# Kernel optimization log

Hardware: AMD Instinct MI355X
Metric: run time of the kernel (lower is better)

The kernel has to match this reference:

```python
import jax, jax.numpy as jnp
import numpy as np

B, S, H = 2, 2048, 512
N, D = 8, 64
EPS = 1e-6


def setup_inputs() -> dict:
    key = jax.random.key(0)
    ks = jax.random.split(key, 8)
    scale = 0.02
    return {
        "query": jax.random.normal(ks[0], (B, S, H), jnp.float32),
        "key": jax.random.normal(ks[1], (B, S, H), jnp.float32),
        "value": jax.random.normal(ks[2], (B, S, H), jnp.float32),
        "wq": jax.random.normal(ks[3], (H, N, D), jnp.float32) * scale,
        "bq": jnp.zeros((N, D), jnp.float32),
        "wk": jax.random.normal(ks[4], (H, N, D), jnp.float32) * scale,
        "bk": jnp.zeros((N, D), jnp.float32),
        "wv": jax.random.normal(ks[5], (H, N, D), jnp.float32) * scale,
        "bv": jnp.zeros((N, D), jnp.float32),
        "wo": jax.random.normal(ks[6], (N, D, H), jnp.float32) * scale,
        "bo": jnp.zeros((H,), jnp.float32),
        "step": 0,
    }


def _feature_map(x):
    # elu(x) + 1 (positive feature map for linear attention)
    return jax.nn.elu(x) + 1.0


def reference(query, key, value, wq, bq, wk, bk, wv, bv, wo, bo, step):
    # QKV projections: [B,S,H] -> [B,S,N,D]
    q = jnp.einsum('bsh,hnd->bsnd', query, wq) + bq
    k = jnp.einsum('bsh,hnd->bsnd', key, wk) + bk
    v = jnp.einsum('bsh,hnd->bsnd', value, wv) + bv

    phi_q = _feature_map(q)
    phi_k = _feature_map(k)

    b, s, n, d = k.shape
    # fold batch & heads: [S, B*N, D]
    pq = phi_q.transpose(1, 0, 2, 3).reshape(s, b * n, d)
    pk = phi_k.transpose(1, 0, 2, 3).reshape(s, b * n, d)
    vv = v.transpose(1, 0, 2, 3).reshape(s, b * n, d)

    # causal linear attention via prefix sums
    # state: cumulative sum of outer products phi_k v^T -> [S, B*N, D, D]
    st = jnp.cumsum(jnp.einsum('sbh,sbd->sbhd', pk, vv), axis=0)
    qs = jnp.einsum('sbhd,sbh->sbd', st, pq)
    z = jnp.cumsum(pk, axis=0)
    qz = jnp.einsum('sbh,sbh->sb', pq, z) + EPS
    a_v = qs / qz[..., None]
    a_v = a_v.transpose(1, 0, 2).reshape(b, s, n, d)

    # output projection: [B,S,N,D] -> [B,S,H]
    return jnp.einsum('bsnd,ndh->bsh', a_v, wo) + bo
```

## Files before the change

kernel.cpp:

```cpp
#include <hip/hip_runtime.h>
#include <hip/hip_bf16.h>
#include <cstdint>

#define B_    2
#define S_    2048
#define H_    512
#define N_    8
#define D_    64
#define BS_   4096
#define CHUNK 64
#define NCH   32
#define NBN   16
#define EPS_  1e-6f

typedef __attribute__((ext_vector_type(4))) float  f32x4;
typedef __attribute__((ext_vector_type(8))) short  short8;
typedef __attribute__((ext_vector_type(4))) short  short4_t;

static __device__ __forceinline__ unsigned short f2bf(float x) {
    __hip_bfloat16 h = __float2bfloat16(x);
    return *reinterpret_cast<unsigned short*>(&h);
}
static __device__ __forceinline__ float bf2f(unsigned short u) {
    unsigned int v = ((unsigned int)u) << 16;
    float f;
    __builtin_memcpy(&f, &v, 4);
    return f;
}

__global__ __launch_bounds__(256) void convert_act_kernel(
    const float* __restrict__ q, const float* __restrict__ k, const float* __restrict__ v,
    unsigned short* __restrict__ qb, unsigned short* __restrict__ kb, unsigned short* __restrict__ vb)
{
    const int p = blockIdx.y;
    const float* src = (p == 0) ? q : (p == 1) ? k : v;
    unsigned short* dst = (p == 0) ? qb : (p == 1) ? kb : vb;
    size_t idx = ((size_t)blockIdx.x * 256 + threadIdx.x) * 8;
    float4 a = *reinterpret_cast<const float4*>(src + idx);
    float4 b = *reinterpret_cast<const float4*>(src + idx + 4);
    short8 o;
    o[0] = (short)f2bf(a.x); o[1] = (short)f2bf(a.y);
    o[2] = (short)f2bf(a.z); o[3] = (short)f2bf(a.w);
    o[4] = (short)f2bf(b.x); o[5] = (short)f2bf(b.y);
    o[6] = (short)f2bf(b.z); o[7] = (short)f2bf(b.w);
    *reinterpret_cast<short8*>(dst + idx) = o;
}

__global__ __launch_bounds__(256) void convert_wt_kernel(
    const float* __restrict__ wq, const float* __restrict__ wk,
    const float* __restrict__ wv, const float* __restrict__ wo,
    unsigned short* __restrict__ wqt, unsigned short* __restrict__ wkt,
    unsigned short* __restrict__ wvt, unsigned short* __restrict__ wot)
{
    const int m = blockIdx.z;
    const float* W = (m == 0) ? wq : (m == 1) ? wk : (m == 2) ? wv : wo;
    unsigned short* Wt = (m == 0) ? wqt : (m == 1) ? wkt : (m == 2) ? wvt : wot;

    __shared__ float t[64][65];
    const int k0 = blockIdx.y * 64, c0 = blockIdx.x * 64;
    const int tid = threadIdx.x;
    const int rr = tid >> 6;
    const int cc = tid & 63;
#pragma unroll
    for (int p = 0; p < 16; p++) {
        int kl = rr + p * 4;
        t[kl][cc] = W[(size_t)(k0 + kl) * 512 + c0 + cc];
    }
    __syncthreads();
#pragma unroll
    for (int p = 0; p < 16; p++) {
        int cl = rr + p * 4;
        Wt[(size_t)(c0 + cl) * 512 + k0 + cc] = f2bf(t[cc][cl]);
    }
}

template<int MODE>
__device__ __forceinline__ void mfma_gemm_body(
    const unsigned short* __restrict__ X, const unsigned short* __restrict__ Wt,
    const float* __restrict__ bias,
    unsigned short* __restrict__ Obf, unsigned short* __restrict__ Ot,
    float* __restrict__ Of)
{
    __shared__ unsigned short As[128][72];
    __shared__ unsigned short Bs[128][72];

    const int tid  = threadIdx.x;
    const int lane = tid & 63;
    const int w    = tid >> 6;
    const int wm   = (w & 1) * 64;
    const int wn   = (w >> 1) * 64;
    const int row0 = blockIdx.y * 128;
    const int col0 = blockIdx.x * 128;
    const int frow = lane & 15;
    const int fk   = (lane >> 4) * 8;

    f32x4 acc[4][4];
#pragma unroll
    for (int m = 0; m < 4; m++)
#pragma unroll
        for (int n = 0; n < 4; n++) acc[m][n] = (f32x4){0.f, 0.f, 0.f, 0.f};

    const int lr = tid >> 3;
    const int lc = (tid & 7) * 8;

    for (int k0 = 0; k0 < 512; k0 += 64) {
#pragma unroll
        for (int p = 0; p < 4; p++) {
            int r = lr + p * 32;
            *reinterpret_cast<short8*>(&As[r][lc]) =
                *reinterpret_cast<const short8*>(X + (size_t)(row0 + r) * 512 + k0 + lc);
            *reinterpret_cast<short8*>(&Bs[r][lc]) =
                *reinterpret_cast<const short8*>(Wt + (size_t)(col0 + r) * 512 + k0 + lc);
        }
        __syncthreads();
#pragma unroll
        for (int kk = 0; kk < 64; kk += 32) {
            short8 a[4], b[4];
#pragma unroll
            for (int m = 0; m < 4; m++)
                a[m] = *reinterpret_cast<const short8*>(&As[wm + m * 16 + frow][kk + fk]);
#pragma unroll
            for (int n = 0; n < 4; n++)
                b[n] = *reinterpret_cast<const short8*>(&Bs[wn + n * 16 + frow][kk + fk]);
#pragma unroll
            for (int m = 0; m < 4; m++)
#pragma unroll
                for (int n = 0; n < 4; n++)
                    acc[m][n] = __builtin_amdgcn_mfma_f32_16x16x32_bf16(
                        a[m], b[n], acc[m][n], 0, 0, 0);
        }
        __syncthreads();
    }

#pragma unroll
    for (int n = 0; n < 4; n++) {
        int col = col0 + wn + n * 16 + frow;
        float bv_ = bias[col];
#pragma unroll
        for (int m = 0; m < 4; m++) {
            int rbase = row0 + wm + m * 16 + (lane >> 4) * 4;
            short4_t t4;
#pragma unroll
            for (int r = 0; r < 4; r++) {
                float val = acc[m][n][r] + bv_;
                if (MODE == 0 || MODE == 1)
                    val = (val > 0.f) ? (val + 1.f) : __expf(val);
                if (MODE == 3) {
                    Of[(size_t)(rbase + r) * 512 + col] = val;
                } else {
                    unsigned short ub = f2bf(val);
                    t4[r] = (short)ub;
                    if (MODE == 0 || MODE == 1)
                        Obf[(size_t)(rbase + r) * 512 + col] = ub;
                }
            }
            if (MODE == 1 || MODE == 2) {
                int bb = rbase >> 11;
                int t_ = rbase & 2047;
                *reinterpret_cast<short4_t*>(
                    Ot + (size_t)bb * (512 * 2048) + (size_t)col * 2048 + t_) = t4;
            }
        }
    }
}

__global__ __launch_bounds__(256) void qkv_proj_kernel(
    const unsigned short* __restrict__ qb, const unsigned short* __restrict__ kb,
    const unsigned short* __restrict__ vb,
    const unsigned short* __restrict__ wqt, const unsigned short* __restrict__ wkt,
    const unsigned short* __restrict__ wvt,
    const float* __restrict__ bq, const float* __restrict__ bk, const float* __restrict__ bv,
    unsigned short* __restrict__ pq, unsigned short* __restrict__ pk,
    unsigned short* __restrict__ pkT, unsigned short* __restrict__ pvT)
{
    int m = blockIdx.z;
    if (m == 0)      mfma_gemm_body<0>(qb, wqt, bq, pq, nullptr, nullptr);
    else if (m == 1) mfma_gemm_body<1>(kb, wkt, bk, pk, pkT, nullptr);
    else             mfma_gemm_body<2>(vb, wvt, bv, nullptr, pvT, nullptr);
}

__global__ __launch_bounds__(256) void out_proj_kernel(
    const unsigned short* __restrict__ avb, const unsigned short* __restrict__ wot,
    const float* __restrict__ bo, float* __restrict__ out)
{
    mfma_gemm_body<3>(avb, wot, bo, nullptr, nullptr, out);
}

__global__ __launch_bounds__(256) void chunk_kv_kernel(
    const unsigned short* __restrict__ pkT, const unsigned short* __restrict__ pvT,
    float* __restrict__ Mb, float* __restrict__ zb)
{
    __shared__ unsigned short KT[64][72];
    __shared__ unsigned short VT[64][72];
    const int c = blockIdx.x, bn = blockIdx.y;
    const int b = bn >> 3, n = bn & 7;
    const int t0 = c * 64;
    const int col0 = n * 64;
    const size_t base_b = (size_t)b * 512 * 2048;
    const int tid = threadIdx.x;
    const int lane = tid & 63, w = tid >> 6;

#pragma unroll
    for (int p = 0; p < 2; p++) {
        int r  = (tid >> 3) + p * 32;
        int c8 = (tid & 7) * 8;
        size_t g = base_b + (size_t)(col0 + r) * 2048 + t0 + c8;
        *reinterpret_cast<short8*>(&KT[r][c8]) = *reinterpret_cast<const short8*>(pkT + g);
        *reinterpret_cast<short8*>(&VT[r][c8]) = *reinterpret_cast<const short8*>(pvT + g);
    }
    __syncthreads();

    const int frow = lane & 15, grp = lane >> 4, fk = grp * 8;
    f32x4 acc[4];
#pragma unroll
    for (int nf = 0; nf < 4; nf++) acc[nf] = (f32x4){0.f, 0.f, 0.f, 0.f};

#pragma unroll
    for (int ks = 0; ks < 2; ks++) {
        short8 a = *reinterpret_cast<const short8*>(&VT[w * 16 + frow][ks * 32 + fk]);
#pragma unroll
        for (int nf = 0; nf < 4; nf++) {
            short8 bfr = *reinterpret_cast<const short8*>(&KT[nf * 16 + frow][ks * 32 + fk]);
            acc[nf] = __builtin_amdgcn_mfma_f32_16x16x32_bf16(a, bfr, acc[nf], 0, 0, 0);
        }
    }

    size_t mbase = ((size_t)bn * NCH + c) * 4096;
#pragma unroll
    for (int nf = 0; nf < 4; nf++)
#pragma unroll
        for (int r = 0; r < 4; r++) {
            int d = w * 16 + grp * 4 + r;
            Mb[mbase + (size_t)d * 64 + nf * 16 + frow] = acc[nf][r];
        }

    if (tid < 64) {
        float s = 0.f;
        for (int t = 0; t < 64; t++) s += bf2f(KT[tid][t]);
        zb[((size_t)bn * NCH + c) * 64 + tid] = s;
    }
}

__global__ __launch_bounds__(256) void scan_kernel(float* __restrict__ Mb,
                                                   float* __restrict__ zb)
{
    const int bn  = blockIdx.y;
    const int tid = threadIdx.x;
    if (blockIdx.x < 16) {
        const int e = blockIdx.x * 256 + tid;
        float run = 0.f;
        for (int c = 0; c < NCH; c++) {
            size_t idx = ((size_t)bn * NCH + c) * 4096 + e;
            float t = Mb[idx];
            Mb[idx] = run;
            run += t;
        }
    } else if (tid < 64) {
        float run = 0.f;
        for (int c = 0; c < NCH; c++) {
            size_t idx = ((size_t)bn * NCH + c) * 64 + tid;
            float t = zb[idx];
            zb[idx] = run;
            run += t;
        }
    }
}

__global__ __launch_bounds__(256) void chunk_attn_kernel(
    const unsigned short* __restrict__ pq, const unsigned short* __restrict__ pk,
    const unsigned short* __restrict__ pvT, const float* __restrict__ Mb,
    const float* __restrict__ zb, unsigned short* __restrict__ av)
{
    __shared__ unsigned short Qs[64][72], Ks[64][72], VT[64][72], SpT[64][72], Ab[64][72];
    __shared__ float zs[64], dQZ[64], dAS[64];

    const int c = blockIdx.x, bn = blockIdx.y;
    const int b = bn >> 3, n = bn & 7;
    const int row0 = b * S_ + c * 64;
    const int col0 = n * 64;
    const int t0 = c * 64;
    const size_t vbase = (size_t)b * 512 * 2048;
    const size_t mbase = ((size_t)bn * NCH + c) * 4096;
    const int tid = threadIdx.x, lane = tid & 63, w = tid >> 6;

#pragma unroll
    for (int p = 0; p < 2; p++) {
        int r  = (tid >> 3) + p * 32;
        int c8 = (tid & 7) * 8;
        *reinterpret_cast<short8*>(&Qs[r][c8]) =
            *reinterpret_cast<const short8*>(pq + (size_t)(row0 + r) * 512 + col0 + c8);
        *reinterpret_cast<short8*>(&Ks[r][c8]) =
            *reinterpret_cast<const short8*>(pk + (size_t)(row0 + r) * 512 + col0 + c8);
        *reinterpret_cast<short8*>(&VT[r][c8]) =
            *reinterpret_cast<const short8*>(pvT + vbase + (size_t)(col0 + r) * 2048 + t0 + c8);
    }
#pragma unroll
    for (int p = 0; p < 16; p++) {
        int i = p * 256 + tid;
        SpT[i >> 6][i & 63] = f2bf(Mb[mbase + i]);
    }
    if (tid < 64) zs[tid] = zb[((size_t)bn * NCH + c) * 64 + tid];
    __syncthreads();

    const int frow = lane & 15, grp = lane >> 4, fk = grp * 8;
    const int srow = w * 16;

    f32x4 a1[4];
#pragma unroll
    for (int tf = 0; tf < 4; tf++) a1[tf] = (f32x4){0.f, 0.f, 0.f, 0.f};
#pragma unroll
    for (int ks = 0; ks < 2; ks++) {
        short8 qa = *reinterpret_cast<const short8*>(&Qs[srow + frow][ks * 32 + fk]);
#pragma unroll
        for (int tf = 0; tf < 4; tf++) {
            short8 kb = *reinterpret_cast<const short8*>(&Ks[tf * 16 + frow][ks * 32 + fk]);
            a1[tf] = __builtin_amdgcn_mfma_f32_16x16x32_bf16(qa, kb, a1[tf], 0, 0, 0);
        }
    }

    float rs[4] = {0.f, 0.f, 0.f, 0.f};
#pragma unroll
    for (int tf = 0; tf < 4; tf++) {
        int t_ = tf * 16 + frow;
#pragma unroll
        for (int r = 0; r < 4; r++) {
            int s_ = srow + grp * 4 + r;
            float v = (t_ <= s_) ? a1[tf][r] : 0.f;
            rs[r] += v;
            Ab[s_][t_] = f2bf(v);
        }
    }
#pragma unroll
    for (int msk = 1; msk < 16; msk <<= 1)
#pragma unroll
        for (int r = 0; r < 4; r++) rs[r] += __shfl_xor(rs[r], msk);
    if (frow == 0) {
#pragma unroll
        for (int r = 0; r < 4; r++) dAS[srow + grp * 4 + r] = rs[r];
    }

    if (tid < 64) {
        float s = 0.f;
        for (int h = 0; h < 64; h++) s += bf2f(Qs[tid][h]) * zs[h];
        dQZ[tid] = s;
    }
    __syncthreads();

    f32x4 o[4];
#pragma unroll
    for (int df = 0; df < 4; df++) o[df] = (f32x4){0.f, 0.f, 0.f, 0.f};
#pragma unroll
    for (int ks = 0; ks < 2; ks++) {
        short8 aa = *reinterpret_cast<const short8*>(&Ab[srow + frow][ks * 32 + fk]);
        short8 qa = *reinterpret_cast<const short8*>(&Qs[srow + frow][ks * 32 + fk]);
#pragma unroll
        for (int df = 0; df < 4; df++) {
            short8 vb = *reinterpret_cast<const short8*>(&VT[df * 16 + frow][ks * 32 + fk]);
            short8 sp = *reinterpret_cast<const short8*>(&SpT[df * 16 + frow][ks * 32 + fk]);
            o[df] = __builtin_amdgcn_mfma_f32_16x16x32_bf16(aa, vb, o[df], 0, 0, 0);
            o[df] = __builtin_amdgcn_mfma_f32_16x16x32_bf16(qa, sp, o[df], 0, 0, 0);
        }
    }

    float inv[4];
    size_t obase[4];
#pragma unroll
    for (int r = 0; r < 4; r++) {
        int s_loc = srow + grp * 4 + r;
        inv[r] = 1.f / (dQZ[s_loc] + dAS[s_loc] + EPS_);
        int s_b = c * 64 + s_loc;
        int jj  = n * S_ + s_b;
        obase[r] = (size_t)(b * S_ + (jj >> 3)) * 512 + (size_t)(jj & 7) * 64;
    }
#pragma unroll
    for (int df = 0; df < 4; df++) {
        int d = df * 16 + frow;
#pragma unroll
        for (int r = 0; r < 4; r++)
            av[obase[r] + d] = f2bf(o[df][r] * inv[r]);
    }
}

extern "C" void kernel_launch(void* const* d_in, const int* in_sizes, int n_in,
                              void* d_out, int out_size, void* d_ws, size_t ws_size,
                              hipStream_t stream)
{
    const float* q_in = (const float*)d_in[0];
    const float* k_in = (const float*)d_in[1];
    const float* v_in = (const float*)d_in[2];
    const float* wq   = (const float*)d_in[3];
    const float* bq   = (const float*)d_in[4];
    const float* wk   = (const float*)d_in[5];
    const float* bk   = (const float*)d_in[6];
    const float* wv   = (const float*)d_in[7];
    const float* bv   = (const float*)d_in[8];
    const float* wo   = (const float*)d_in[9];
    const float* bo   = (const float*)d_in[10];
    float* out = (float*)d_out;

    const size_t PLANE = (size_t)BS_ * 512;

    float* ws = (float*)d_ws;
    float* Mb   = ws;
    float* zbuf = Mb + PLANE;
    unsigned short* u16 = (unsigned short*)(zbuf + 32768);
    unsigned short* qb  = u16;
    unsigned short* kb  = qb  + PLANE;
    unsigned short* vb  = kb  + PLANE;
    unsigned short* pq  = vb  + PLANE;
    unsigned short* pk  = pq  + PLANE;
    unsigned short* pkT = pk  + PLANE;
    unsigned short* pvT = pkT + PLANE;
    unsigned short* avb = pvT + PLANE;
    unsigned short* wqt = avb + PLANE;
    unsigned short* wkt = wqt + 262144;
    unsigned short* wvt = wkt + 262144;
    unsigned short* wot = wvt + 262144;

    convert_act_kernel<<<dim3(1024, 3), 256, 0, stream>>>(q_in, k_in, v_in, qb, kb, vb);
    convert_wt_kernel<<<dim3(8, 8, 4), 256, 0, stream>>>(wq, wk, wv, wo, wqt, wkt, wvt, wot);
    qkv_proj_kernel<<<dim3(4, 32, 3), 256, 0, stream>>>(
        qb, kb, vb, wqt, wkt, wvt, bq, bk, bv, pq, pk, pkT, pvT);
    chunk_kv_kernel<<<dim3(NCH, NBN), 256, 0, stream>>>(pkT, pvT, Mb, zbuf);
    scan_kernel<<<dim3(17, NBN), 256, 0, stream>>>(Mb, zbuf);
    chunk_attn_kernel<<<dim3(NCH, NBN), 256, 0, stream>>>(pq, pk, pvT, Mb, zbuf, avb);
    out_proj_kernel<<<dim3(4, 32), 256, 0, stream>>>(avb, wot, bo, out);
}
```

Baseline: 157.8 us.

## Fuse activation conversion into QKV GEMM, merge chunk-state and scan kernels

Drops the separate fp32-to-bf16 activation conversion kernel; the QKV GEMM now loads fp32 inputs and converts them while staging into shared memory. GEMM tiles shrink from 128x128 to 128x64, doubling the block count for better CU occupancy. The per-chunk KV outer-product kernel and the serial scan kernel are merged into one kernel that computes running prefix states per wave with MFMA and combines wave totals through shared memory. The q·z dot product in the attention kernel is spread across all 256 threads instead of 64. Costs include redundant fp32 loads across column blocks in the GEMM and a more complex scan layout.

```diff
diff --git a/kernel.cpp b/kernel.cpp
--- a/kernel.cpp
+++ b/kernel.cpp
@@ -28,24 +28,6 @@
     return f;
 }
 
-__global__ __launch_bounds__(256) void convert_act_kernel(
-    const float* __restrict__ q, const float* __restrict__ k, const float* __restrict__ v,
-    unsigned short* __restrict__ qb, unsigned short* __restrict__ kb, unsigned short* __restrict__ vb)
-{
-    const int p = blockIdx.y;
-    const float* src = (p == 0) ? q : (p == 1) ? k : v;
-    unsigned short* dst = (p == 0) ? qb : (p == 1) ? kb : vb;
-    size_t idx = ((size_t)blockIdx.x * 256 + threadIdx.x) * 8;
-    float4 a = *reinterpret_cast<const float4*>(src + idx);
-    float4 b = *reinterpret_cast<const float4*>(src + idx + 4);
-    short8 o;
-    o[0] = (short)f2bf(a.x); o[1] = (short)f2bf(a.y);
-    o[2] = (short)f2bf(a.z); o[3] = (short)f2bf(a.w);
-    o[4] = (short)f2bf(b.x); o[5] = (short)f2bf(b.y);
-    o[6] = (short)f2bf(b.z); o[7] = (short)f2bf(b.w);
-    *reinterpret_cast<short8*>(dst + idx) = o;
-}
-
 __global__ __launch_bounds__(256) void convert_wt_kernel(
     const float* __restrict__ wq, const float* __restrict__ wk,
     const float* __restrict__ wv, const float* __restrict__ wo,
@@ -76,29 +58,29 @@
 
 template<int MODE>
 __device__ __forceinline__ void mfma_gemm_body(
-    const unsigned short* __restrict__ X, const unsigned short* __restrict__ Wt,
+    const void* __restrict__ Xv, const unsigned short* __restrict__ Wt,
     const float* __restrict__ bias,
     unsigned short* __restrict__ Obf, unsigned short* __restrict__ Ot,
     float* __restrict__ Of)
 {
     __shared__ unsigned short As[128][72];
-    __shared__ unsigned short Bs[128][72];
+    __shared__ unsigned short Bs[64][72];
 
     const int tid  = threadIdx.x;
     const int lane = tid & 63;
     const int w    = tid >> 6;
     const int wm   = (w & 1) * 64;
-    const int wn   = (w >> 1) * 64;
+    const int wn   = (w >> 1) * 32;
     const int row0 = blockIdx.y * 128;
-    const int col0 = blockIdx.x * 128;
+    const int col0 = blockIdx.x * 64;
     const int frow = lane & 15;
     const int fk   = (lane >> 4) * 8;
 
-    f32x4 acc[4][4];
+    f32x4 acc[4][2];
 #pragma unroll
     for (int m = 0; m < 4; m++)
 #pragma unroll
-        for (int n = 0; n < 4; n++) acc[m][n] = (f32x4){0.f, 0.f, 0.f, 0.f};
+        for (int n = 0; n < 2; n++) acc[m][n] = (f32x4){0.f, 0.f, 0.f, 0.f};
 
     const int lr = tid >> 3;
     const int lc = (tid & 7) * 8;
@@ -107,25 +89,43 @@
 #pragma unroll
         for (int p = 0; p < 4; p++) {
             int r = lr + p * 32;
-            *reinterpret_cast<short8*>(&As[r][lc]) =
-                *reinterpret_cast<const short8*>(X + (size_t)(row0 + r) * 512 + k0 + lc);
+            if (MODE == 3) {
+                const unsigned short* X = (const unsigned short*)Xv;
+                *reinterpret_cast<short8*>(&As[r][lc]) =
+                    *reinterpret_cast<const short8*>(X + (size_t)(row0 + r) * 512 + k0 + lc);
+            } else {
+                const float* X = (const float*)Xv;
+                const float* src = X + (size_t)(row0 + r) * 512 + k0 + lc;
+                float4 x0 = *reinterpret_cast<const float4*>(src);
+                float4 x1 = *reinterpret_cast<const float4*>(src + 4);
+                short8 o;
+                o[0] = (short)f2bf(x0.x); o[1] = (short)f2bf(x0.y);
+                o[2] = (short)f2bf(x0.z); o[3] = (short)f2bf(x0.w);
+                o[4] = (short)f2bf(x1.x); o[5] = (short)f2bf(x1.y);
+                o[6] = (short)f2bf(x1.z); o[7] = (short)f2bf(x1.w);
+                *reinterpret_cast<short8*>(&As[r][lc]) = o;
+            }
+        }
+#pragma unroll
+        for (int p = 0; p < 2; p++) {
+            int r = (tid >> 3) + p * 32;
             *reinterpret_cast<short8*>(&Bs[r][lc]) =
                 *reinterpret_cast<const short8*>(Wt + (size_t)(col0 + r) * 512 + k0 + lc);
         }
         __syncthreads();
 #pragma unroll
         for (int kk = 0; kk < 64; kk += 32) {
-            short8 a[4], b[4];
+            short8 a[4], b[2];
 #pragma unroll
             for (int m = 0; m < 4; m++)
                 a[m] = *reinterpret_cast<const short8*>(&As[wm + m * 16 + frow][kk + fk]);
 #pragma unroll
-            for (int n = 0; n < 4; n++)
+            for (int n = 0; n < 2; n++)
                 b[n] = *reinterpret_cast<const short8*>(&Bs[wn + n * 16 + frow][kk + fk]);
 #pragma unroll
             for (int m = 0; m < 4; m++)
 #pragma unroll
-                for (int n = 0; n < 4; n++)
+                for (int n = 0; n < 2; n++)
                     acc[m][n] = __builtin_amdgcn_mfma_f32_16x16x32_bf16(
                         a[m], b[n], acc[m][n], 0, 0, 0);
         }
@@ -133,7 +133,7 @@
     }
 
 #pragma unroll
-    for (int n = 0; n < 4; n++) {
+    for (int n = 0; n < 2; n++) {
         int col = col0 + wn + n * 16 + frow;
         float bv_ = bias[col];
 #pragma unroll
@@ -165,8 +165,8 @@
 }
 
 __global__ __launch_bounds__(256) void qkv_proj_kernel(
-    const unsigned short* __restrict__ qb, const unsigned short* __restrict__ kb,
-    const unsigned short* __restrict__ vb,
+    const float* __restrict__ q_in, const float* __restrict__ k_in,
+    const float* __restrict__ v_in,
     const unsigned short* __restrict__ wqt, const unsigned short* __restrict__ wkt,
     const unsigned short* __restrict__ wvt,
     const float* __restrict__ bq, const float* __restrict__ bk, const float* __restrict__ bv,
@@ -174,9 +174,9 @@
     unsigned short* __restrict__ pkT, unsigned short* __restrict__ pvT)
 {
     int m = blockIdx.z;
-    if (m == 0)      mfma_gemm_body<0>(qb, wqt, bq, pq, nullptr, nullptr);
-    else if (m == 1) mfma_gemm_body<1>(kb, wkt, bk, pk, pkT, nullptr);
-    else             mfma_gemm_body<2>(vb, wvt, bv, nullptr, pvT, nullptr);
+    if (m == 0)      mfma_gemm_body<0>(q_in, wqt, bq, pq, nullptr, nullptr);
+    else if (m == 1) mfma_gemm_body<1>(k_in, wkt, bk, pk, pkT, nullptr);
+    else             mfma_gemm_body<2>(v_in, wvt, bv, nullptr, pvT, nullptr);
 }
 
 __global__ __launch_bounds__(256) void out_proj_kernel(
@@ -186,83 +186,73 @@
     mfma_gemm_body<3>(avb, wot, bo, nullptr, nullptr, out);
 }
 
-__global__ __launch_bounds__(256) void chunk_kv_kernel(
+__global__ __launch_bounds__(256) void chunk_kvscan_kernel(
     const unsigned short* __restrict__ pkT, const unsigned short* __restrict__ pvT,
     float* __restrict__ Mb, float* __restrict__ zb)
 {
-    __shared__ unsigned short KT[64][72];
-    __shared__ unsigned short VT[64][72];
-    const int c = blockIdx.x, bn = blockIdx.y;
+    __shared__ float waveTot[4][256];
+    __shared__ float zTot[4][16];
+
+    const int tile = blockIdx.x;
+    const int bn   = blockIdx.y;
+    const int d0   = (tile >> 2) * 16;
+    const int h0   = (tile & 3) * 16;
     const int b = bn >> 3, n = bn & 7;
-    const int t0 = c * 64;
-    const int col0 = n * 64;
-    const size_t base_b = (size_t)b * 512 * 2048;
-    const int tid = threadIdx.x;
-    const int lane = tid & 63, w = tid >> 6;
-
-#pragma unroll
-    for (int p = 0; p < 2; p++) {
-        int r  = (tid >> 3) + p * 32;
-        int c8 = (tid & 7) * 8;
-        size_t g = base_b + (size_t)(col0 + r) * 2048 + t0 + c8;
-        *reinterpret_cast<short8*>(&KT[r][c8]) = *reinterpret_cast<const short8*>(pkT + g);
-        *reinterpret_cast<short8*>(&VT[r][c8]) = *reinterpret_cast<const short8*>(pvT + g);
-    }
+    const int tid = threadIdx.x, lane = tid & 63, w = tid >> 6;
+    const int frow = lane & 15, grp = lane >> 4, fk = grp * 8;
+    const bool do_z = (tile >> 2) == 0;
+
+    const size_t vrow = (size_t)b * (512 * 2048) + (size_t)(n * 64 + d0 + frow) * 2048;
+    const size_t krow = (size_t)b * (512 * 2048) + (size_t)(n * 64 + h0 + frow) * 2048;
+
+    f32x4 run = (f32x4){0.f, 0.f, 0.f, 0.f};
+    f32x4 loc[8];
+    float runz = 0.f, locz[8];
+
+#pragma unroll
+    for (int c = 0; c < 8; c++) {
+        int t0 = (w * 8 + c) * 64;
+        loc[c] = run;
+        locz[c] = runz;
+        short8 a0 = *reinterpret_cast<const short8*>(pvT + vrow + t0 + fk);
+        short8 a1 = *reinterpret_cast<const short8*>(pvT + vrow + t0 + 32 + fk);
+        short8 b0 = *reinterpret_cast<const short8*>(pkT + krow + t0 + fk);
+        short8 b1 = *reinterpret_cast<const short8*>(pkT + krow + t0 + 32 + fk);
+        run = __builtin_amdgcn_mfma_f32_16x16x32_bf16(a0, b0, run, 0, 0, 0);
+        run = __builtin_amdgcn_mfma_f32_16x16x32_bf16(a1, b1, run, 0, 0, 0);
+        if (do_z) {
+            float zp = 0.f;
+#pragma unroll
+            for (int j = 0; j < 8; j++) zp += bf2f((unsigned short)b0[j]) + bf2f((unsigned short)b1[j]);
+            zp += __shfl_xor(zp, 16);
+            zp += __shfl_xor(zp, 32);
+            runz += zp;
+        }
+    }
+
+#pragma unroll
+    for (int r = 0; r < 4; r++)
+        waveTot[w][(grp * 4 + r) * 16 + frow] = run[r];
+    if (do_z && lane < 16) zTot[w][frow] = runz;
     __syncthreads();
 
-    const int frow = lane & 15, grp = lane >> 4, fk = grp * 8;
-    f32x4 acc[4];
-#pragma unroll
-    for (int nf = 0; nf < 4; nf++) acc[nf] = (f32x4){0.f, 0.f, 0.f, 0.f};
-
-#pragma unroll
-    for (int ks = 0; ks < 2; ks++) {
-        short8 a = *reinterpret_cast<const short8*>(&VT[w * 16 + frow][ks * 32 + fk]);
-#pragma unroll
-        for (int nf = 0; nf < 4; nf++) {
-            short8 bfr = *reinterpret_cast<const short8*>(&KT[nf * 16 + frow][ks * 32 + fk]);
-            acc[nf] = __builtin_amdgcn_mfma_f32_16x16x32_bf16(a, bfr, acc[nf], 0, 0, 0);
-        }
-    }
-
-    size_t mbase = ((size_t)bn * NCH + c) * 4096;
-#pragma unroll
-    for (int nf = 0; nf < 4; nf++)
-#pragma unroll
-        for (int r = 0; r < 4; r++) {
-            int d = w * 16 + grp * 4 + r;
-            Mb[mbase + (size_t)d * 64 + nf * 16 + frow] = acc[nf][r];
-        }
-
-    if (tid < 64) {
-        float s = 0.f;
-        for (int t = 0; t < 64; t++) s += bf2f(KT[tid][t]);
-        zb[((size_t)bn * NCH + c) * 64 + tid] = s;
-    }
-}
-
-__global__ __launch_bounds__(256) void scan_kernel(float* __restrict__ Mb,
-                                                   float* __restrict__ zb)
-{
-    const int bn  = blockIdx.y;
-    const int tid = threadIdx.x;
-    if (blockIdx.x < 16) {
-        const int e = blockIdx.x * 256 + tid;
-        float run = 0.f;
-        for (int c = 0; c < NCH; c++) {
-            size_t idx = ((size_t)bn * NCH + c) * 4096 + e;
-            float t = Mb[idx];
-            Mb[idx] = run;
-            run += t;
-        }
-    } else if (tid < 64) {
-        float run = 0.f;
-        for (int c = 0; c < NCH; c++) {
-            size_t idx = ((size_t)bn * NCH + c) * 64 + tid;
-            float t = zb[idx];
-            zb[idx] = run;
-            run += t;
-        }
+    f32x4 carry = (f32x4){0.f, 0.f, 0.f, 0.f};
+    float carryz = 0.f;
+    for (int pw = 0; pw < w; pw++) {
+#pragma unroll
+        for (int r = 0; r < 4; r++)
+            carry[r] += waveTot[pw][(grp * 4 + r) * 16 + frow];
+        carryz += zTot[pw][frow];
+    }
+
+#pragma unroll
+    for (int c = 0; c < 8; c++) {
+        size_t mbase = ((size_t)bn * NCH + (w * 8 + c)) * 4096;
+#pragma unroll
+        for (int r = 0; r < 4; r++)
+            Mb[mbase + (size_t)(d0 + grp * 4 + r) * 64 + h0 + frow] = carry[r] + loc[c][r];
+        if (do_z && lane < 16)
+            zb[((size_t)bn * NCH + (w * 8 + c)) * 64 + h0 + frow] = carryz + locz[c];
     }
 }
 
@@ -272,7 +262,7 @@
     const float* __restrict__ zb, unsigned short* __restrict__ av)
 {
     __shared__ unsigned short Qs[64][72], Ks[64][72], VT[64][72], SpT[64][72], Ab[64][72];
-    __shared__ float zs[64], dQZ[64], dAS[64];
+    __shared__ float zs[64], dqz4[64][4], dAS[64];
 
     const int c = blockIdx.x, bn = blockIdx.y;
     const int b = bn >> 3, n = bn & 7;
@@ -339,10 +329,15 @@
         for (int r = 0; r < 4; r++) dAS[srow + grp * 4 + r] = rs[r];
     }
 
-    if (tid < 64) {
-        float s = 0.f;
-        for (int h = 0; h < 64; h++) s += bf2f(Qs[tid][h]) * zs[h];
-        dQZ[tid] = s;
+    {
+        int s = tid & 63, part = tid >> 6;
+        float sdq = 0.f;
+#pragma unroll
+        for (int j = 0; j < 16; j++) {
+            int h = part * 16 + j;
+            sdq += bf2f(Qs[s][h]) * zs[h];
+        }
+        dqz4[s][part] = sdq;
     }
     __syncthreads();
 
@@ -367,7 +362,8 @@
 #pragma unroll
     for (int r = 0; r < 4; r++) {
         int s_loc = srow + grp * 4 + r;
-        inv[r] = 1.f / (dQZ[s_loc] + dAS[s_loc] + EPS_);
+        float dq = dqz4[s_loc][0] + dqz4[s_loc][1] + dqz4[s_loc][2] + dqz4[s_loc][3];
+        inv[r] = 1.f / (dq + dAS[s_loc] + EPS_);
         int s_b = c * 64 + s_loc;
         int jj  = n * S_ + s_b;
         obase[r] = (size_t)(b * S_ + (jj >> 3)) * 512 + (size_t)(jj & 7) * 64;
@@ -404,10 +400,7 @@
     float* Mb   = ws;
     float* zbuf = Mb + PLANE;
     unsigned short* u16 = (unsigned short*)(zbuf + 32768);
-    unsigned short* qb  = u16;
-    unsigned short* kb  = qb  + PLANE;
-    unsigned short* vb  = kb  + PLANE;
-    unsigned short* pq  = vb  + PLANE;
+    unsigned short* pq  = u16;
     unsigned short* pk  = pq  + PLANE;
     unsigned short* pkT = pk  + PLANE;
     unsigned short* pvT = pkT + PLANE;
@@ -417,12 +410,10 @@
     unsigned short* wvt = wkt + 262144;
     unsigned short* wot = wvt + 262144;
 
-    convert_act_kernel<<<dim3(1024, 3), 256, 0, stream>>>(q_in, k_in, v_in, qb, kb, vb);
     convert_wt_kernel<<<dim3(8, 8, 4), 256, 0, stream>>>(wq, wk, wv, wo, wqt, wkt, wvt, wot);
-    qkv_proj_kernel<<<dim3(4, 32, 3), 256, 0, stream>>>(
-        qb, kb, vb, wqt, wkt, wvt, bq, bk, bv, pq, pk, pkT, pvT);
-    chunk_kv_kernel<<<dim3(NCH, NBN), 256, 0, stream>>>(pkT, pvT, Mb, zbuf);
-    scan_kernel<<<dim3(17, NBN), 256, 0, stream>>>(Mb, zbuf);
+    qkv_proj_kernel<<<dim3(8, 32, 3), 256, 0, stream>>>(
+        q_in, k_in, v_in, wqt, wkt, wvt, bq, bk, bv, pq, pk, pkT, pvT);
+    chunk_kvscan_kernel<<<dim3(16, NBN), 256, 0, stream>>>(pkT, pvT, Mb, zbuf);
     chunk_attn_kernel<<<dim3(NCH, NBN), 256, 0, stream>>>(pq, pk, pvT, Mb, zbuf, avb);
-    out_proj_kernel<<<dim3(4, 32), 256, 0, stream>>>(avb, wot, bo, out);
-}
+    out_proj_kernel<<<dim3(8, 32), 256, 0, stream>>>(avb, wot, bo, out);
+}
```

After: 155.4 us. About the same (-1.5%).
